# Performance work log

Measured on AMD Instinct MI355X. Metric: run time of the kernel, lower is better.

## Reference

```python
import jax, jax.numpy as jnp
import numpy as np

TAU = 20.0   # membrane time constant (init default)
TH = 1.0     # spike threshold (init default)
K = 10.0     # surrogate sigmoid slope (hard-coded in forward)
EPS = 1e-6


def setup_inputs() -> dict:
    key = jax.random.key(0)
    I = jax.random.normal(key, (4096, 4096), dtype=jnp.float32)  # [B, L]
    return {"I": I}


def reference(I):
    B, L = I.shape

    def step(v, I_t):
        # Euler: dv = -v/tau + I ; v <- v + dv
        v = v - v / TAU + I_t
        s_soft = jax.nn.sigmoid(K * (v - TH))
        s_hard = (v >= TH).astype(I.dtype)
        # straight-through: value = s_hard, gradient flows through s_soft
        s = jax.lax.stop_gradient(s_hard - s_soft) + s_soft
        # reset: v <- v * (1 - stopgrad(s)); stopgrad(s) has value s_hard
        v = v * (1.0 - s_hard)
        return v, (s, s_hard)

    v0 = jnp.zeros((B,), dtype=I.dtype)
    _, (spikes_t, hard_t) = jax.lax.scan(step, v0, I.T)  # xs: [L, B]
    spikes = spikes_t.T       # [B, L]
    hard_spikes = hard_t.T    # [B, L]

    # hard latency: index of first hard spike, else L
    fired = hard_spikes > 0.5
    has = jnp.any(fired, axis=1)
    idx = jnp.argmax(fired, axis=1)
    hard_latency = jnp.where(has, idx, L).astype(jnp.int32)  # [B]

    # soft latency: spike-weighted mean time
    time = jnp.arange(L, dtype=spikes.dtype)
    w = spikes / (spikes.sum(axis=1, keepdims=True) + EPS)
    soft_latency = (w * time).sum(axis=1)  # [B]

    return spikes, hard_latency, soft_latency
```

## Files before the change

### kernel.cpp

```cpp
#include <hip/hip_runtime.h>

#define B_DIM 4096
#define L_DIM 4096
#define SEGLEN 256
#define NSEG (L_DIM / SEGLEN)
#define WARM 512
#define CHUNK 64
#define LROW 64

typedef __attribute__((ext_vector_type(4))) float f32x4;

#define LIF_CORE(IIN)                         \
    float q0 = u * cdiv;                      \
    float rr = fmaf(-20.0f, q0, u);           \
    float q  = fmaf(rr, cdiv, q0);            \
    float a  = u - q;                        \
    float b  = a + (IIN);                     \
    u = sp ? (IIN) : b;                       \
    sp = (u >= 1.0f);

#define WARM_STEP(IIN) { LIF_CORE(IIN) }

#define FULL_STEP(IIN, SOUT)                  \
    {                                         \
        LIF_CORE(IIN)                         \
        float sf = sp ? 1.0f : 0.0f;          \
        cnt += sf;                            \
        seen = fmaxf(seen, sf);               \
        accS += cnt;                          \
        accF += seen;                         \
        (SOUT) = sf;                          \
    }

typedef const __attribute__((address_space(1))) void g_void;
typedef __attribute__((address_space(3))) void l_void;
__device__ __forceinline__ void gll16(const float* src, float* ldsbase) {
    __builtin_amdgcn_global_load_lds((g_void*)src, (l_void*)ldsbase, 16, 0, 0);
}

__global__ __launch_bounds__(128, 1) void lif_kernel(const float* __restrict__ I,
                                                     float* __restrict__ out,
                                                     float* __restrict__ Cacc,
                                                     float* __restrict__ tsAcc,
                                                     int* __restrict__ firstAcc) {
    __shared__ __align__(16) float lds[2][2][64 * LROW];
    const int wid = threadIdx.x >> 6;
    const int lane = threadIdx.x & 63;
    float* buf0 = &lds[wid][0][0];
    float* buf1 = &lds[wid][1][0];

    const int rowBase = (blockIdx.x >> 3) * 64;
    const int seg = ((blockIdx.x & 7) << 1) + wid;
    const int t0 = seg * SEGLEN;
    const int start = (t0 > WARM) ? (t0 - WARM) : 0;
    const int nwarmCh = (t0 - start) / CHUNK;
    const int nch = nwarmCh + SEGLEN / CHUNK;

    const int srow = lane >> 4, scol = lane & 15;
    const float* gbase = I + (size_t)rowBase * L_DIM + start;

    const int row = rowBase + lane;
    float u = 0.f, cnt = 0.f, seen = 0.f, accS = 0.f, accF = 0.f;
    bool sp = false;
    const float cdiv = 0.05f;
    float4 R[16];

#define GLL_CHUNK(CC, DST)                                                  \
    {                                                                       \
        const float* gsrc = gbase + (size_t)(CC) * CHUNK;                   \
        _Pragma("unroll")                                                   \
        for (int p = 0; p < 16; ++p) {                                      \
            const int r = 4 * p + srow;                                     \
            gll16(gsrc + (size_t)r * L_DIM + (((scol - r) & 15) << 2),      \
                  (DST) + p * 256);                                         \
        }                                                                   \
    }

#define READ_R(SRC)                                                         \
    {                                                                       \
        _Pragma("unroll")                                                   \
        for (int j = 0; j < 16; ++j)                                        \
            R[j] = *(const float4*)&(SRC)[lane * LROW + (((j + lane) & 15) << 2)]; \
    }

    GLL_CHUNK(0, buf0)
    asm volatile("s_waitcnt vmcnt(0)" ::: "memory");
    __builtin_amdgcn_sched_barrier(0);
    READ_R(buf0)

    for (int c = 0; c < nch; ++c) {
        float* bufc = (c & 1) ? buf1 : buf0;
        float* bufn = (c & 1) ? buf0 : buf1;

        if (c + 1 < nch) GLL_CHUNK(c + 1, bufn)
        __builtin_amdgcn_sched_barrier(0);

        if (c < nwarmCh) {
#pragma unroll
            for (int j = 0; j < 16; ++j) {
                float4 iv = R[j];
                WARM_STEP(iv.x) WARM_STEP(iv.y) WARM_STEP(iv.z) WARM_STEP(iv.w)
            }
        } else {
#pragma unroll
            for (int j = 0; j < 16; ++j) {
                float4 iv = R[j];
                float4 sv;
                FULL_STEP(iv.x, sv.x) FULL_STEP(iv.y, sv.y)
                FULL_STEP(iv.z, sv.z) FULL_STEP(iv.w, sv.w)
                *(float4*)&bufc[lane * LROW + (((j + lane) & 15) << 2)] = sv;
            }
            f32x4 S[16];
#pragma unroll
            for (int p = 0; p < 16; ++p)
                S[p] = *(const f32x4*)&bufc[p * 256 + lane * 4];
            float* og = out + (size_t)rowBase * L_DIM + t0 +
                        (size_t)(c - nwarmCh) * CHUNK;
#pragma unroll
            for (int p = 0; p < 16; ++p) {
                const int r = 4 * p + srow;
                __builtin_nontemporal_store(
                    S[p], (f32x4*)(og + (size_t)r * L_DIM + (((scol - r) & 15) << 2)));
            }
        }

        if (c + 1 < nch) {
            if (c >= nwarmCh) {
                asm volatile("s_waitcnt vmcnt(16)" ::: "memory");
            } else {
                asm volatile("s_waitcnt vmcnt(0)" ::: "memory");
            }
            __builtin_amdgcn_sched_barrier(0);
            READ_R(bufn)
        }
    }

    if (cnt > 0.f) {
        const int firstLocal = (int)((float)SEGLEN - accF);
        atomicMin(&firstAcc[row], t0 + firstLocal);
    }
    atomicAdd(&Cacc[row], cnt);
    atomicAdd(&tsAcc[row], fmaf((float)(t0 + SEGLEN), cnt, -accS));
#undef GLL_CHUNK
#undef READ_R
}

__global__ __launch_bounds__(256) void fin_kernel(const float* __restrict__ Cacc,
                                                  const float* __restrict__ tsAcc,
                                                  const int* __restrict__ firstAcc,
                                                  float* __restrict__ out) {
    int r = blockIdx.x * 256 + threadIdx.x;
    if (r < B_DIM) {
        int f = firstAcc[r];
        out[(size_t)B_DIM * L_DIM + r] = (float)(f > L_DIM ? L_DIM : f);
        out[(size_t)B_DIM * L_DIM + B_DIM + r] = tsAcc[r] / (Cacc[r] + 1e-6f);
    }
}

extern "C" void kernel_launch(void* const* d_in, const int* in_sizes, int n_in,
                              void* d_out, int out_size, void* d_ws, size_t ws_size,
                              hipStream_t stream) {
    const float* I = (const float*)d_in[0];
    float* out = (float*)d_out;
    float* wsf = (float*)d_ws;
    int* wsi = (int*)((float*)d_ws + 2 * B_DIM);
    (void)in_sizes; (void)n_in; (void)out_size; (void)ws_size;

    (void)hipMemsetAsync(wsf, 0, 2 * B_DIM * sizeof(float), stream);
    (void)hipMemsetAsync(wsi, 0x7F, B_DIM * sizeof(int), stream);
    lif_kernel<<<(B_DIM / 64) * (NSEG / 2), 128, 0, stream>>>(I, out, wsf, wsf + B_DIM, wsi);
    fin_kernel<<<(B_DIM + 255) / 256, 256, 0, stream>>>(wsf, wsf + B_DIM, wsi, out);
}
```

Before: 134.0 us.

## Double chunk size and make each wave process two segments persistently

Chunk width grows from 64 to 128 timesteps, so LDS becomes 128KB per block and each lane holds 32 float4 registers. The grid is cut to 256 blocks, each looping over two segments per wave, with a block-to-row/segment remap that puts consecutive blocks on different row groups. The aim is fewer, larger DMA batches per chunk and roughly one block per CU, cutting launch-tail and scheduling overhead. In exchange register pressure rises, each wave runs more serial work, and the warmup recompute per segment stays the same.

After: 227.9 us. 70.1% more time.

```diff
diff --git a/kernel.cpp b/kernel.cpp
--- a/kernel.cpp
+++ b/kernel.cpp
@@ -5,8 +5,8 @@
 #define SEGLEN 256
 #define NSEG (L_DIM / SEGLEN)
 #define WARM 512
-#define CHUNK 64
-#define LROW 64
+#define CHUNK 128
+#define LROW 128
 
 typedef __attribute__((ext_vector_type(4))) float f32x4;
 
@@ -14,7 +14,7 @@
     float q0 = u * cdiv;                      \
     float rr = fmaf(-20.0f, q0, u);           \
     float q  = fmaf(rr, cdiv, q0);            \
-    float a  = u - q;                        \
+    float a  = u - q;                         \
     float b  = a + (IIN);                     \
     u = sp ? (IIN) : b;                       \
     sp = (u >= 1.0f);
@@ -38,6 +38,8 @@
     __builtin_amdgcn_global_load_lds((g_void*)src, (l_void*)ldsbase, 16, 0, 0);
 }
 
+static_assert(2 * 2 * 64 * LROW * sizeof(float) == 131072, "LDS geometry");
+
 __global__ __launch_bounds__(128, 1) void lif_kernel(const float* __restrict__ I,
                                                      float* __restrict__ out,
                                                      float* __restrict__ Cacc,
@@ -49,29 +51,21 @@
     float* buf0 = &lds[wid][0][0];
     float* buf1 = &lds[wid][1][0];
 
-    const int rowBase = (blockIdx.x >> 3) * 64;
-    const int seg = ((blockIdx.x & 7) << 1) + wid;
-    const int t0 = seg * SEGLEN;
-    const int start = (t0 > WARM) ? (t0 - WARM) : 0;
-    const int nwarmCh = (t0 - start) / CHUNK;
-    const int nch = nwarmCh + SEGLEN / CHUNK;
+    const int rowBase = (blockIdx.x & 63) * 64;
+    const int segA = ((blockIdx.x >> 6) << 1) + wid;
 
-    const int srow = lane >> 4, scol = lane & 15;
-    const float* gbase = I + (size_t)rowBase * L_DIM + start;
+    const int srow = lane >> 5, scol = lane & 31;
+    const int row = rowBase + lane;
+    const float* Ibase = I + (size_t)rowBase * L_DIM;
+    const float cdiv = 0.05f;
 
-    const int row = rowBase + lane;
-    float u = 0.f, cnt = 0.f, seen = 0.f, accS = 0.f, accF = 0.f;
-    bool sp = false;
-    const float cdiv = 0.05f;
-    float4 R[16];
-
-#define GLL_CHUNK(CC, DST)                                                  \
+#define GLL_CHUNK(GB, CC, DST)                                              \
     {                                                                       \
-        const float* gsrc = gbase + (size_t)(CC) * CHUNK;                   \
+        const float* gsrc = (GB) + (size_t)(CC) * CHUNK;                    \
         _Pragma("unroll")                                                   \
-        for (int p = 0; p < 16; ++p) {                                      \
-            const int r = 4 * p + srow;                                     \
-            gll16(gsrc + (size_t)r * L_DIM + (((scol - r) & 15) << 2),      \
+        for (int p = 0; p < 32; ++p) {                                      \
+            const int r = 2 * p + srow;                                     \
+            gll16(gsrc + (size_t)r * L_DIM + (((scol - r) & 31) << 2),      \
                   (DST) + p * 256);                                         \
         }                                                                   \
     }
@@ -79,68 +73,95 @@
 #define READ_R(SRC)                                                         \
     {                                                                       \
         _Pragma("unroll")                                                   \
-        for (int j = 0; j < 16; ++j)                                        \
-            R[j] = *(const float4*)&(SRC)[lane * LROW + (((j + lane) & 15) << 2)]; \
+        for (int j = 0; j < 32; ++j)                                        \
+            R[j] = *(const float4*)&(SRC)[lane * LROW + (((j + lane) & 31) << 2)]; \
     }
 
-    GLL_CHUNK(0, buf0)
-    asm volatile("s_waitcnt vmcnt(0)" ::: "memory");
-    __builtin_amdgcn_sched_barrier(0);
-    READ_R(buf0)
+    for (int task = 0; task < 2; ++task) {
+        const int seg = segA + 8 * task;
+        const int t0 = seg * SEGLEN;
+        const int start = (t0 > WARM) ? (t0 - WARM) : 0;
+        const int nwarmCh = (t0 - start) / CHUNK;
+        const int nch = nwarmCh + SEGLEN / CHUNK;
+        const float* gbase = Ibase + start;
 
-    for (int c = 0; c < nch; ++c) {
-        float* bufc = (c & 1) ? buf1 : buf0;
-        float* bufn = (c & 1) ? buf0 : buf1;
+        float u = 0.f, cnt = 0.f, seen = 0.f, accS = 0.f, accF = 0.f;
+        bool sp = false;
+        float4 R[32];
 
-        if (c + 1 < nch) GLL_CHUNK(c + 1, bufn)
+        GLL_CHUNK(gbase, 0, buf0)
+        asm volatile("s_waitcnt vmcnt(0)" ::: "memory");
         __builtin_amdgcn_sched_barrier(0);
+        READ_R(buf0)
 
-        if (c < nwarmCh) {
+        for (int c = 0; c < nch; ++c) {
+            float* bufc = (c & 1) ? buf1 : buf0;
+            float* bufn = (c & 1) ? buf0 : buf1;
+
+            if (c + 1 < nch) GLL_CHUNK(gbase, c + 1, bufn)
+            __builtin_amdgcn_sched_barrier(0);
+
+            if (c < nwarmCh) {
 #pragma unroll
-            for (int j = 0; j < 16; ++j) {
-                float4 iv = R[j];
-                WARM_STEP(iv.x) WARM_STEP(iv.y) WARM_STEP(iv.z) WARM_STEP(iv.w)
+                for (int j = 0; j < 32; ++j) {
+                    float4 iv = R[j];
+                    WARM_STEP(iv.x) WARM_STEP(iv.y) WARM_STEP(iv.z) WARM_STEP(iv.w)
+                }
+            } else {
+#pragma unroll
+                for (int j = 0; j < 32; ++j) {
+                    float4 iv = R[j];
+                    float4 sv;
+                    FULL_STEP(iv.x, sv.x) FULL_STEP(iv.y, sv.y)
+                    FULL_STEP(iv.z, sv.z) FULL_STEP(iv.w, sv.w)
+                    *(float4*)&bufc[lane * LROW + (((j + lane) & 31) << 2)] = sv;
+                }
+                float* og = out + (size_t)rowBase * L_DIM + t0 +
+                            (size_t)(c - nwarmCh) * CHUNK;
+                {
+                    f32x4 S0[16];
+#pragma unroll
+                    for (int p = 0; p < 16; ++p)
+                        S0[p] = *(const f32x4*)&bufc[p * 256 + lane * 4];
+#pragma unroll
+                    for (int p = 0; p < 16; ++p) {
+                        const int r = 2 * p + srow;
+                        __builtin_nontemporal_store(
+                            S0[p], (f32x4*)(og + (size_t)r * L_DIM + (((scol - r) & 31) << 2)));
+                    }
+                }
+                {
+                    f32x4 S1[16];
+#pragma unroll
+                    for (int p = 0; p < 16; ++p)
+                        S1[p] = *(const f32x4*)&bufc[(p + 16) * 256 + lane * 4];
+#pragma unroll
+                    for (int p = 0; p < 16; ++p) {
+                        const int r = 2 * (p + 16) + srow;
+                        __builtin_nontemporal_store(
+                            S1[p], (f32x4*)(og + (size_t)r * L_DIM + (((scol - r) & 31) << 2)));
+                    }
+                }
             }
-        } else {
-#pragma unroll
-            for (int j = 0; j < 16; ++j) {
-                float4 iv = R[j];
-                float4 sv;
-                FULL_STEP(iv.x, sv.x) FULL_STEP(iv.y, sv.y)
-                FULL_STEP(iv.z, sv.z) FULL_STEP(iv.w, sv.w)
-                *(float4*)&bufc[lane * LROW + (((j + lane) & 15) << 2)] = sv;
-            }
-            f32x4 S[16];
-#pragma unroll
-            for (int p = 0; p < 16; ++p)
-                S[p] = *(const f32x4*)&bufc[p * 256 + lane * 4];
-            float* og = out + (size_t)rowBase * L_DIM + t0 +
-                        (size_t)(c - nwarmCh) * CHUNK;
-#pragma unroll
-            for (int p = 0; p < 16; ++p) {
-                const int r = 4 * p + srow;
-                __builtin_nontemporal_store(
-                    S[p], (f32x4*)(og + (size_t)r * L_DIM + (((scol - r) & 15) << 2)));
+
+            if (c + 1 < nch) {
+                if (c >= nwarmCh) {
+                    asm volatile("s_waitcnt vmcnt(32)" ::: "memory");
+                } else {
+                    asm volatile("s_waitcnt vmcnt(0)" ::: "memory");
+                }
+                __builtin_amdgcn_sched_barrier(0);
+                READ_R(bufn)
             }
         }
 
-        if (c + 1 < nch) {
-            if (c >= nwarmCh) {
-                asm volatile("s_waitcnt vmcnt(16)" ::: "memory");
-            } else {
-                asm volatile("s_waitcnt vmcnt(0)" ::: "memory");
-            }
-            __builtin_amdgcn_sched_barrier(0);
-            READ_R(bufn)
+        if (cnt > 0.f) {
+            const int firstLocal = (int)((float)SEGLEN - accF);
+            atomicMin(&firstAcc[row], t0 + firstLocal);
         }
+        atomicAdd(&Cacc[row], cnt);
+        atomicAdd(&tsAcc[row], fmaf((float)(t0 + SEGLEN), cnt, -accS));
     }
-
-    if (cnt > 0.f) {
-        const int firstLocal = (int)((float)SEGLEN - accF);
-        atomicMin(&firstAcc[row], t0 + firstLocal);
-    }
-    atomicAdd(&Cacc[row], cnt);
-    atomicAdd(&tsAcc[row], fmaf((float)(t0 + SEGLEN), cnt, -accS));
 #undef GLL_CHUNK
 #undef READ_R
 }
@@ -168,6 +189,6 @@
 
     (void)hipMemsetAsync(wsf, 0, 2 * B_DIM * sizeof(float), stream);
     (void)hipMemsetAsync(wsi, 0x7F, B_DIM * sizeof(int), stream);
-    lif_kernel<<<(B_DIM / 64) * (NSEG / 2), 128, 0, stream>>>(I, out, wsf, wsf + B_DIM, wsi);
+    lif_kernel<<<256, 128, 0, stream>>>(I, out, wsf, wsf + B_DIM, wsi);
     fin_kernel<<<(B_DIM + 255) / 256, 256, 0, stream>>>(wsf, wsf + B_DIM, wsi, out);
 }
```
